# Kernel optimization log

Measured on AMD Instinct MI355X. Metric: run time of the kernel, lower is better.

## Reference

```python
import jax, jax.numpy as jnp
import numpy as np

B = 8192
D = 512          # hidden_dim
OBS_EMB = 256
COMM = 128
N_ACT = 4
N_LAYERS = 2
D_INNER = 2 * D
D_STATE = 16
DT_RANK = D // 16  # 32
D_CONV = 4
EPS = 1e-5


def _xavier(k, shape):
    s = jnp.sqrt(2.0 / (shape[-2] + shape[-1]))
    return jax.random.normal(k, shape, jnp.float32) * s


def setup_inputs() -> dict:
    ks = jax.random.split(jax.random.key(0), 16)
    p = {}
    p['obs'] = jax.random.normal(ks[0], (B, 75), jnp.float32)
    p['comm_in'] = jax.random.normal(ks[1], (B, COMM), jnp.float32)
    # obs encoder: Conv2d(3->32, k=3, valid) + Linear(288->256)
    p['conv_w'] = jax.random.normal(ks[2], (32, 3, 3, 3), jnp.float32) * jnp.sqrt(2.0 / 27.0)
    p['conv_b'] = jnp.zeros((32,), jnp.float32)
    p['enc_w'] = _xavier(ks[3], (288, OBS_EMB))
    p['enc_b'] = jnp.zeros((OBS_EMB,), jnp.float32)
    p['proj_w'] = _xavier(ks[4], (OBS_EMB + COMM, D))
    p['proj_b'] = jnp.zeros((D,), jnp.float32)
    # Mamba stack params (stacked over layers)
    p['norm_w'] = jnp.ones((N_LAYERS, D), jnp.float32)
    p['in_proj_w'] = _xavier(ks[5], (N_LAYERS, D, 2 * D_INNER))
    p['conv1d_w'] = jax.random.normal(ks[6], (N_LAYERS, D_INNER, D_CONV), jnp.float32) / jnp.sqrt(D_CONV)
    p['conv1d_b'] = jnp.zeros((N_LAYERS, D_INNER), jnp.float32)
    p['x_proj_w'] = _xavier(ks[7], (N_LAYERS, D_INNER, DT_RANK + 2 * D_STATE))
    p['dt_proj_w'] = _xavier(ks[8], (N_LAYERS, DT_RANK, D_INNER))
    p['dt_proj_b'] = jnp.full((N_LAYERS, D_INNER), jnp.log(jnp.expm1(0.01)), jnp.float32)  # dt ~ 0.01
    p['A_log'] = jnp.log(jnp.broadcast_to(jnp.arange(1, D_STATE + 1, dtype=jnp.float32), (N_LAYERS, D_INNER, D_STATE)))
    p['D_param'] = jnp.ones((N_LAYERS, D_INNER), jnp.float32)
    p['out_proj_w'] = _xavier(ks[9], (N_LAYERS, D_INNER, D))
    p['final_norm_w'] = jnp.ones((D,), jnp.float32)
    # output heads
    p['act_w'] = _xavier(ks[10], (D, N_ACT)); p['act_b'] = jnp.zeros((N_ACT,), jnp.float32)
    p['comm_w'] = _xavier(ks[11], (D, COMM)); p['comm_b'] = jnp.zeros((COMM,), jnp.float32)
    p['val_w'] = _xavier(ks[12], (D, 1)); p['val_b'] = jnp.zeros((1,), jnp.float32)
    return p


def _rmsnorm(x, w):
    return x * jax.lax.rsqrt(jnp.mean(x * x, axis=-1, keepdims=True) + EPS) * w


def _mamba_block(u, Wi, cw, cb, Wx, Wdt, bdt, Alog, Dp, Wo):
    # u: (B, L, D) -> (B, L, D)
    Bsz, L, _ = u.shape
    d_inner = Dp.shape[0]
    x, z = jnp.split(u @ Wi, 2, axis=-1)                       # (B,L,di) each
    # causal depthwise conv1d over L
    xt = jnp.pad(jnp.swapaxes(x, 1, 2), ((0, 0), (0, 0), (D_CONV - 1, 0)))
    xc = jax.lax.conv_general_dilated(xt, cw[:, None, :], (1,), 'VALID',
                                      feature_group_count=d_inner,
                                      dimension_numbers=('NCH', 'OIH', 'NCH'))
    x = jax.nn.silu(jnp.swapaxes(xc, 1, 2) + cb)
    x_dbl = x @ Wx                                              # (B,L,dt_rank+2*ns)
    dt = jax.nn.softplus(x_dbl[..., :DT_RANK] @ Wdt + bdt)      # (B,L,di)
    Bm = x_dbl[..., DT_RANK:DT_RANK + D_STATE]                  # (B,L,ns)
    Cm = x_dbl[..., DT_RANK + D_STATE:]                         # (B,L,ns)
    A = -jnp.exp(Alog)                                          # (di,ns)
    dA = jnp.exp(dt[..., None] * A)                             # (B,L,di,ns)
    dBx = dt[..., None] * Bm[:, :, None, :] * x[..., None]      # (B,L,di,ns)

    def step(h, inp):
        dA_t, dBx_t, C_t = inp
        h = dA_t * h + dBx_t
        return h, jnp.einsum('bds,bs->bd', h, C_t)

    h0 = jnp.zeros((Bsz, d_inner, D_STATE), u.dtype)
    _, ys = jax.lax.scan(step, h0, (jnp.swapaxes(dA, 0, 1), jnp.swapaxes(dBx, 0, 1), jnp.swapaxes(Cm, 0, 1)))
    y = jnp.swapaxes(ys, 0, 1) + x * Dp
    return (y * jax.nn.silu(z)) @ Wo


def reference(obs, comm_in, conv_w, conv_b, enc_w, enc_b, proj_w, proj_b,
              norm_w, in_proj_w, conv1d_w, conv1d_b, x_proj_w, dt_proj_w, dt_proj_b,
              A_log, D_param, out_proj_w, final_norm_w,
              act_w, act_b, comm_w, comm_b, val_w, val_b):
    Bsz = obs.shape[0]
    v = obs.reshape(Bsz, 3, 5, 5)
    v = jax.lax.conv_general_dilated(v, conv_w, (1, 1), 'VALID',
                                     dimension_numbers=('NCHW', 'OIHW', 'NCHW'))
    v = jax.nn.relu(v + conv_b[None, :, None, None]).reshape(Bsz, -1)   # (B,288)
    emb = jax.nn.relu(v @ enc_w + enc_b)                                 # (B,256)
    x = jax.nn.relu(jnp.concatenate([emb, comm_in], axis=-1) @ proj_w + proj_b)  # (B,512)
    h = x[:, None, :]                                                    # (B, L=1, D)
    for i in range(norm_w.shape[0]):
        h = h + _mamba_block(_rmsnorm(h, norm_w[i]), in_proj_w[i], conv1d_w[i],
                             conv1d_b[i], x_proj_w[i], dt_proj_w[i], dt_proj_b[i],
                             A_log[i], D_param[i], out_proj_w[i])
    h = _rmsnorm(h, final_norm_w)[:, 0, :]
    action_logits = h @ act_w + act_b
    comm_out = jnp.tanh(h @ comm_w + comm_b)
    value = h @ val_w + val_b
    return action_logits, comm_out, value
```

## Files before the change

kernel.cpp:

```cpp
#include <hip/hip_runtime.h>
#include <math.h>


typedef __bf16 bf16x8 __attribute__((ext_vector_type(8)));
typedef float f32x4 __attribute__((ext_vector_type(4)));
typedef short short8 __attribute__((ext_vector_type(8)));
typedef short short4v __attribute__((ext_vector_type(4)));

__device__ __forceinline__ float siluf(float v){ return v / (1.f + __expf(-v)); }
__device__ __forceinline__ float spfast(float v){ return v > 15.f ? v : __logf(1.f + __expf(v)); }
__device__ __forceinline__ float b2f(unsigned short u){ return __uint_as_float(((unsigned)u)<<16); }
__device__ __forceinline__ unsigned short f2b(float f){
  unsigned u = __float_as_uint(f);
  return (unsigned short)((u + 0x7fffu + ((u>>16)&1u)) >> 16);
}
__device__ __forceinline__ void g2l16(const void* g, void* l){
  __builtin_amdgcn_global_load_lds((const __attribute__((address_space(1))) unsigned int*)g,
                                   (__attribute__((address_space(3))) unsigned int*)l, 16, 0, 0);
}

__global__ __launch_bounds__(256) void k_wt_all(
    const float* __restrict__ in_proj_w, const float* __restrict__ out_proj_w,
    const float* __restrict__ x_proj_w,  const float* __restrict__ dt_proj_w,
    const float* __restrict__ enc_w,     const float* __restrict__ proj_w,
    const float* __restrict__ act_w, const float* __restrict__ comm_w, const float* __restrict__ val_w,
    const float* __restrict__ obs, const float* __restrict__ comm_in,
    const float* __restrict__ conv_w, const float* __restrict__ conv_b,
    unsigned short* __restrict__ wi_t, unsigned short* __restrict__ wo_t,
    unsigned short* __restrict__ wx_t, unsigned short* __restrict__ wdt_t,
    unsigned short* __restrict__ we_t, unsigned short* __restrict__ wp_t,
    unsigned short* __restrict__ wh_t,
    unsigned short* __restrict__ v, unsigned short* __restrict__ cat)
{
  int b = blockIdx.x;
  const int t = threadIdx.x;

  if (b >= 3792) {
    __shared__ float s_obs[8][76];
    const int r0 = (b - 3792) * 8;
    for (int i = t; i < 8*75; i += 256) s_obs[i/75][i%75] = obs[(size_t)(r0 + i/75)*75 + i%75];
    __syncthreads();
    for (int i = t; i < 8*288; i += 256) {
      int r = i / 288, o = i % 288;
      int c = o / 9, ij = o % 9, oi = ij/3, oj = ij%3;
      float acc = conv_b[c];
      #pragma unroll
      for (int ic=0; ic<3; ic++)
        #pragma unroll
        for (int ki=0; ki<3; ki++)
          #pragma unroll
          for (int kj=0; kj<3; kj++)
            acc = fmaf(s_obs[r][ic*25 + (oi+ki)*5 + (oj+kj)], conv_w[((c*3+ic)*3+ki)*3+kj], acc);
      v[(size_t)(r0+r)*320 + o] = f2b(fmaxf(acc, 0.f));
    }
    v[(size_t)(r0 + (t>>5))*320 + 288 + (t&31)] = 0;
    for (int i = t; i < 8*128; i += 256) {
      int r = i >> 7, c = i & 127;
      cat[(size_t)(r0+r)*384 + 256 + c] = f2b(comm_in[(size_t)(r0+r)*128 + c]);
    }
    return;
  }
  if (b >= 3536) {
    const int n = b - 3536;
    for (int k = t; k < 512; k += 256) {
      float v2;
      if (n < 4)         v2 = act_w[k*4 + n];
      else if (n < 132)  v2 = comm_w[k*128 + (n-4)];
      else if (n == 132) v2 = val_w[k];
      else               v2 = 0.f;
      wh_t[(size_t)n*512 + k] = f2b(v2);
    }
    return;
  }
  const float* Wsrc; unsigned short* Wdst; int Kd, Nd, KP, nkb;
  if (b < 2048) {
    const int L = b >> 10; b &= 1023;
    Wsrc = in_proj_w + (size_t)L*512*2048; Wdst = wi_t + (size_t)L*2048*512;
    Kd = 512; Nd = 2048; KP = 512; nkb = 16;
  } else if (b < 3072) {
    b -= 2048; const int L = b >> 9; b &= 511;
    Wsrc = out_proj_w + (size_t)L*1024*512; Wdst = wo_t + (size_t)L*512*1024;
    Kd = 1024; Nd = 512; KP = 1024; nkb = 32;
  } else if (b < 3200) {
    b -= 3072; const int L = b >> 6; b &= 63;
    Wsrc = x_proj_w + (size_t)L*1024*64; Wdst = wx_t + (size_t)L*64*1024;
    Kd = 1024; Nd = 64; KP = 1024; nkb = 32;
  } else if (b < 3264) {
    b -= 3200; const int L = b >> 5; b &= 31;
    Wsrc = dt_proj_w + (size_t)L*32*1024; Wdst = wdt_t + (size_t)L*1024*32;
    Kd = 32; Nd = 1024; KP = 32; nkb = 1;
  } else if (b < 3344) {
    b -= 3264; Wsrc = enc_w; Wdst = we_t; Kd = 288; Nd = 256; KP = 320; nkb = 10;
  } else {
    b -= 3344; Wsrc = proj_w; Wdst = wp_t; Kd = 384; Nd = 512; KP = 384; nkb = 12;
  }
  __shared__ float s[32][33];
  const int kb = (b % nkb)*32, nb = (b / nkb)*32;
  const int c = t & 31, r = t >> 5;
  #pragma unroll
  for (int i=0;i<32;i+=8) {
    const int k = kb + r + i;
    s[r+i][c] = (k < Kd) ? Wsrc[(size_t)k*Nd + nb + c] : 0.f;
  }
  __syncthreads();
  #pragma unroll
  for (int i=0;i<32;i+=8) Wdst[(size_t)(nb+r+i)*KP + kb + c] = f2b(s[c][r+i]);
}

__global__ __launch_bounds__(256) void k_rms(const float* __restrict__ h,
                                             const float* __restrict__ nw,
                                             unsigned short* __restrict__ u)
{
  const int l = threadIdx.x & 63;
  const size_t row = (size_t)blockIdx.x*4 + (threadIdx.x>>6);
  const float4* hp = (const float4*)(h + row*512) + l*2;
  float4 v0 = hp[0], v1 = hp[1];
  float ss = v0.x*v0.x+v0.y*v0.y+v0.z*v0.z+v0.w*v0.w
           + v1.x*v1.x+v1.y*v1.y+v1.z*v1.z+v1.w*v1.w;
  #pragma unroll
  for (int m=32;m;m>>=1) ss += __shfl_xor(ss, m, 64);
  const float sc = rsqrtf(ss*(1.f/512.f) + 1e-5f);
  const float4* np = (const float4*)nw + l*2;
  float4 w0 = np[0], w1 = np[1];
  short8 o;
  o[0]=(short)f2b(v0.x*sc*w0.x); o[1]=(short)f2b(v0.y*sc*w0.y);
  o[2]=(short)f2b(v0.z*sc*w0.z); o[3]=(short)f2b(v0.w*sc*w0.w);
  o[4]=(short)f2b(v1.x*sc*w1.x); o[5]=(short)f2b(v1.y*sc*w1.y);
  o[6]=(short)f2b(v1.z*sc*w1.z); o[7]=(short)f2b(v1.w*sc*w1.w);
  *(short8*)(u + row*512 + l*8) = o;
}

template<int K, int NB>
__device__ __forceinline__ void gemmT(const unsigned short* __restrict__ A,
                                      const unsigned short* __restrict__ Bt,
                                      int r0, int c0,
                                      unsigned short* sA, unsigned short* sB,
                                      f32x4 (&acc)[4][NB/32])
{
  constexpr int NF = NB/32;
  const int tid = threadIdx.x;
  const int l = tid & 63;
  const int wr = (tid>>7)&1, wc = (tid>>6)&1;
  const int rowA = tid>>3, kc8 = (tid&7)*8;
  const unsigned short* gA = A  + (size_t)(r0+rowA)*K + kc8;
  const unsigned short* gB = Bt + (size_t)(c0+rowA)*K + kc8;
  const int aOff = (wr*64 + (l&15))*64 + ((l>>4)*8);
  const int bOff = (wc*(NB/2) + (l&15))*64 + ((l>>4)*8);
  for (int kt=0; kt<K; kt+=64) {
    #pragma unroll
    for (int it=0; it<4; ++it) g2l16(gA + (size_t)(it*32)*K + kt, sA + ((it*256+tid)*8));
    #pragma unroll
    for (int it=0; it<NB/32; ++it) g2l16(gB + (size_t)(it*32)*K + kt, sB + ((it*256+tid)*8));
    __syncthreads();
    #pragma unroll
    for (int ks=0; ks<64; ks+=32) {
      bf16x8 af[4], bfm[NF];
      #pragma unroll
      for (int m=0;m<4;m++) af[m]  = *(const bf16x8*)(sA + (m*16)*64 + aOff + ks);
      #pragma unroll
      for (int n=0;n<NF;n++) bfm[n] = *(const bf16x8*)(sB + (n*16)*64 + bOff + ks);
      #pragma unroll
      for (int m=0;m<4;m++)
        #pragma unroll
        for (int n=0;n<NF;n++)
          acc[m][n] = __builtin_amdgcn_mfma_f32_16x16x32_bf16(af[m], bfm[n], acc[m][n], 0, 0, 0);
    }
    __syncthreads();
  }
}

__global__ __launch_bounds__(256) void k_gemm_inproj(
    const unsigned short* __restrict__ A, const unsigned short* __restrict__ Bt,
    const float* __restrict__ cw, const float* __restrict__ cb,
    unsigned short* __restrict__ xs, unsigned short* __restrict__ zs)
{
  __shared__ unsigned short sA[128*64], sB[128*64];
  f32x4 acc[4][4];
  #pragma unroll
  for (int m=0;m<4;m++)
    #pragma unroll
    for (int n=0;n<4;n++) acc[m][n] = (f32x4){0.f,0.f,0.f,0.f};
  const int r0 = blockIdx.x*128, c0 = blockIdx.y*128;
  gemmT<512,128>(A, Bt, r0, c0, sA, sB, acc);

  const int tid = threadIdx.x, l = tid & 63;
  const int wr = (tid>>7)&1, wc = (tid>>6)&1;
  const int colB = c0 + wc*64 + (l&15);
  const int rowB = r0 + wr*64 + ((l>>4)*4);
  if (c0 < 1024) {
    #pragma unroll
    for (int n=0;n<4;n++){
      const int col = colB + n*16;
      const float cw3 = cw[col*4+3], cbv = cb[col];
      #pragma unroll
      for (int m=0;m<4;m++)
        #pragma unroll
        for (int j=0;j<4;j++){
          const int row = rowB + m*16 + j;
          xs[(size_t)row*1024 + col] = f2b(siluf(fmaf(acc[m][n][j], cw3, cbv)));
        }
    }
  } else {
    #pragma unroll
    for (int n=0;n<4;n++){
      const int col = colB + n*16 - 1024;
      #pragma unroll
      for (int m=0;m<4;m++)
        #pragma unroll
        for (int j=0;j<4;j++){
          const int row = rowB + m*16 + j;
          zs[(size_t)row*1024 + col] = f2b(siluf(acc[m][n][j]));
        }
    }
  }
}

__global__ __launch_bounds__(256) void k_gemm_outproj(
    const unsigned short* __restrict__ A, const unsigned short* __restrict__ Bt,
    float* __restrict__ h)
{
  __shared__ unsigned short sA[128*64], sB[64*64];
  f32x4 acc[4][2];
  #pragma unroll
  for (int m=0;m<4;m++)
    #pragma unroll
    for (int n=0;n<2;n++) acc[m][n] = (f32x4){0.f,0.f,0.f,0.f};
  const int r0 = blockIdx.x*128, c0 = blockIdx.y*64;
  gemmT<1024,64>(A, Bt, r0, c0, sA, sB, acc);

  const int tid = threadIdx.x, l = tid & 63;
  const int wr = (tid>>7)&1, wc = (tid>>6)&1;
  const int colB = c0 + wc*32 + (l&15);
  const int rowB = r0 + wr*64 + ((l>>4)*4);
  #pragma unroll
  for (int n=0;n<2;n++){
    const int col = colB + n*16;
    #pragma unroll
    for (int m=0;m<4;m++)
      #pragma unroll
      for (int j=0;j<4;j++){
        const int row = rowB + m*16 + j;
        h[(size_t)row*512 + col] += acc[m][n][j];
      }
  }
}

__global__ __launch_bounds__(256) void k_gemm_enc(
    const unsigned short* __restrict__ A, const unsigned short* __restrict__ Bt,
    const float* __restrict__ bias, unsigned short* __restrict__ cat)
{
  __shared__ unsigned short sA[128*64], sB[64*64];
  f32x4 acc[4][2];
  #pragma unroll
  for (int m=0;m<4;m++)
    #pragma unroll
    for (int n=0;n<2;n++) acc[m][n] = (f32x4){0.f,0.f,0.f,0.f};
  const int r0 = blockIdx.x*128, c0 = blockIdx.y*64;
  gemmT<320,64>(A, Bt, r0, c0, sA, sB, acc);

  const int tid = threadIdx.x, l = tid & 63;
  const int wr = (tid>>7)&1, wc = (tid>>6)&1;
  const int colB = c0 + wc*32 + (l&15);
  const int rowB = r0 + wr*64 + ((l>>4)*4);
  #pragma unroll
  for (int n=0;n<2;n++){
    const int col = colB + n*16;
    const float bv = bias[col];
    #pragma unroll
    for (int m=0;m<4;m++)
      #pragma unroll
      for (int j=0;j<4;j++){
        const size_t row = rowB + m*16 + j;
        cat[row*384 + col] = f2b(fmaxf(acc[m][n][j] + bv, 0.f));
      }
  }
}

__global__ __launch_bounds__(256) void k_gemm_proj(
    const unsigned short* __restrict__ A, const unsigned short* __restrict__ Bt,
    const float* __restrict__ bias, float* __restrict__ h)
{
  __shared__ unsigned short sA[128*64], sB[64*64];
  f32x4 acc[4][2];
  #pragma unroll
  for (int m=0;m<4;m++)
    #pragma unroll
    for (int n=0;n<2;n++) acc[m][n] = (f32x4){0.f,0.f,0.f,0.f};
  const int r0 = blockIdx.x*128, c0 = blockIdx.y*64;
  gemmT<384,64>(A, Bt, r0, c0, sA, sB, acc);

  const int tid = threadIdx.x, l = tid & 63;
  const int wr = (tid>>7)&1, wc = (tid>>6)&1;
  const int colB = c0 + wc*32 + (l&15);
  const int rowB = r0 + wr*64 + ((l>>4)*4);
  #pragma unroll
  for (int n=0;n<2;n++){
    const int col = colB + n*16;
    const float bv = bias[col];
    #pragma unroll
    for (int m=0;m<4;m++)
      #pragma unroll
      for (int j=0;j<4;j++){
        const size_t row = rowB + m*16 + j;
        h[row*512 + col] = fmaxf(acc[m][n][j] + bv, 0.f);
      }
  }
}

__global__ __launch_bounds__(256) void k_gemm_heads(
    const unsigned short* __restrict__ A, const unsigned short* __restrict__ Bt,
    const float* __restrict__ act_b, const float* __restrict__ comm_b,
    const float* __restrict__ val_b, float* __restrict__ out)
{
  __shared__ unsigned short sA[128*64], sB[64*64];
  f32x4 acc[4][2];
  #pragma unroll
  for (int m=0;m<4;m++)
    #pragma unroll
    for (int n=0;n<2;n++) acc[m][n] = (f32x4){0.f,0.f,0.f,0.f};
  const int r0 = blockIdx.x*128, c0 = blockIdx.y*64;
  gemmT<512,64>(A, Bt, r0, c0, sA, sB, acc);

  const int tid = threadIdx.x, l = tid & 63;
  const int wr = (tid>>7)&1, wc = (tid>>6)&1;
  const int colB = c0 + wc*32 + (l&15);
  const int rowB = r0 + wr*64 + ((l>>4)*4);
  #pragma unroll
  for (int n=0;n<2;n++){
    const int col = colB + n*16;
    if (col > 132) continue;
    #pragma unroll
    for (int m=0;m<4;m++)
      #pragma unroll
      for (int j=0;j<4;j++){
        const size_t row = rowB + m*16 + j;
        float v = acc[m][n][j];
        if (col < 4)        out[row*4 + col] = v + act_b[col];
        else if (col < 132) out[32768 + row*128 + (col-4)] = tanhf(v + comm_b[col-4]);
        else                out[1081344 + row] = v + val_b[0];
      }
  }
}

__global__ __launch_bounds__(256) void k_xdbl2(
    const unsigned short* __restrict__ xs, const unsigned short* __restrict__ Wx_t,
    unsigned short* __restrict__ dt_in, float* __restrict__ bc_g)
{
  __shared__ unsigned short sA[32*128];
  __shared__ unsigned short sB[64*128];
  __shared__ float s_dbl[32][64];
  const int tid = threadIdx.x, l = tid & 63, w = tid >> 6;
  const int r0 = blockIdx.x * 32;
  f32x4 acc0 = (f32x4){0.f,0.f,0.f,0.f}, acc1 = (f32x4){0.f,0.f,0.f,0.f};
  for (int kt = 0; kt < 1024; kt += 128) {
    #pragma unroll
    for (int it=0; it<2; ++it) {
      const int idx = it*256 + tid;
      g2l16(xs + (size_t)(r0 + (idx>>4))*1024 + (idx&15)*8 + kt, sA + idx*8);
    }
    #pragma unroll
    for (int it=0; it<4; ++it) {
      const int idx = it*256 + tid;
      g2l16(Wx_t + (size_t)(idx>>4)*1024 + (idx&15)*8 + kt, sB + idx*8);
    }
    __syncthreads();
    #pragma unroll
    for (int ks=0; ks<128; ks+=32) {
      bf16x8 a0 = *(const bf16x8*)(sA + ((l&15))*128      + (l>>4)*8 + ks);
      bf16x8 a1 = *(const bf16x8*)(sA + (16+(l&15))*128   + (l>>4)*8 + ks);
      bf16x8 bf = *(const bf16x8*)(sB + (w*16+(l&15))*128 + (l>>4)*8 + ks);
      acc0 = __builtin_amdgcn_mfma_f32_16x16x32_bf16(a0, bf, acc0, 0, 0, 0);
      acc1 = __builtin_amdgcn_mfma_f32_16x16x32_bf16(a1, bf, acc1, 0, 0, 0);
    }
    __syncthreads();
  }
  #pragma unroll
  for (int j=0;j<4;j++) {
    s_dbl[(l>>4)*4 + j]     [w*16 + (l&15)] = acc0[j];
    s_dbl[16 + (l>>4)*4 + j][w*16 + (l&15)] = acc1[j];
  }
  __syncthreads();
  if (tid < 32) {
    float a = 0.f;
    #pragma unroll
    for (int s=0;s<16;s++) a = fmaf(s_dbl[tid][32+s], s_dbl[tid][48+s], a);
    bc_g[r0 + tid] = a;
  }
  {
    const int r = tid >> 3, c4 = (tid & 7)*4;
    short4v o;
    o[0] = (short)f2b(s_dbl[r][c4]);   o[1] = (short)f2b(s_dbl[r][c4+1]);
    o[2] = (short)f2b(s_dbl[r][c4+2]); o[3] = (short)f2b(s_dbl[r][c4+3]);
    *(short4v*)(dt_in + (size_t)(r0+r)*32 + c4) = o;
  }
}

__global__ __launch_bounds__(256) void k_dtgate2(
    unsigned short* __restrict__ xs, const unsigned short* __restrict__ zs,
    const unsigned short* __restrict__ dt_in, const float* __restrict__ bc_g,
    const unsigned short* __restrict__ Wdt_t,
    const float* __restrict__ bdt, const float* __restrict__ Dp)
{
  __shared__ unsigned short sA[128*32];
  __shared__ unsigned short sB[128*32];
  __shared__ float s_bc[128];
  const int tid = threadIdx.x, l = tid & 63;
  const int r0 = blockIdx.x*128, c0 = blockIdx.y*128;

  { const int row = tid >> 1, kh = (tid & 1)*16;
    const short8* ap = (const short8*)(dt_in + (size_t)(r0+row)*32 + kh);
    *(short8*)(sA + row*32 + kh)     = ap[0];
    *(short8*)(sA + row*32 + kh + 8) = ap[1];
    const short8* wp = (const short8*)(Wdt_t + (size_t)(c0+row)*32 + kh);
    *(short8*)(sB + row*32 + kh)     = wp[0];
    *(short8*)(sB + row*32 + kh + 8) = wp[1];
  }
  if (tid < 128) s_bc[tid] = bc_g[r0 + tid];
  __syncthreads();

  const int wr = (tid>>7)&1, wc = (tid>>6)&1;
  bf16x8 af[4], bfm[4];
  #pragma unroll
  for (int m=0;m<4;m++) af[m]  = *(const bf16x8*)(sA + (wr*64 + m*16 + (l&15))*32 + (l>>4)*8);
  #pragma unroll
  for (int n=0;n<4;n++) bfm[n] = *(const bf16x8*)(sB + (wc*64 + n*16 + (l&15))*32 + (l>>4)*8);
  f32x4 acc[4][4];
  #pragma unroll
  for (int m=0;m<4;m++)
    #pragma unroll
    for (int n=0;n<4;n++)
      acc[m][n] = __builtin_amdgcn_mfma_f32_16x16x32_bf16(af[m], bfm[n], (f32x4){0.f,0.f,0.f,0.f}, 0, 0, 0);

  #pragma unroll
  for (int n=0;n<4;n++){
    const int col = c0 + wc*64 + n*16 + (l&15);
    const float bj = bdt[col], dpj = Dp[col];
    #pragma unroll
    for (int m=0;m<4;m++){
      const int rloc = wr*64 + m*16 + (l>>4)*4;
      #pragma unroll
      for (int j=0;j<4;j++){
        const size_t row = r0 + rloc + j;
        const float dtv = spfast(acc[m][n][j] + bj);
        const float f = fmaf(dtv, s_bc[rloc + j], dpj);
        const float x = b2f(xs[row*1024 + col]);
        const float z = b2f(zs[row*1024 + col]);
        xs[row*1024 + col] = f2b(x * f * z);
      }
    }
  }
}

extern "C" void kernel_launch(void* const* d_in, const int* in_sizes, int n_in,
                              void* d_out, int out_size, void* d_ws, size_t ws_size,
                              hipStream_t stream) {
  const float* obs       = (const float*)d_in[0];
  const float* comm_in   = (const float*)d_in[1];
  const float* conv_w    = (const float*)d_in[2];
  const float* conv_b    = (const float*)d_in[3];
  const float* enc_w     = (const float*)d_in[4];
  const float* enc_b     = (const float*)d_in[5];
  const float* proj_w    = (const float*)d_in[6];
  const float* proj_b    = (const float*)d_in[7];
  const float* norm_w    = (const float*)d_in[8];
  const float* in_proj_w = (const float*)d_in[9];
  const float* conv1d_w  = (const float*)d_in[10];
  const float* conv1d_b  = (const float*)d_in[11];
  const float* x_proj_w  = (const float*)d_in[12];
  const float* dt_proj_w = (const float*)d_in[13];
  const float* dt_proj_b = (const float*)d_in[14];
  const float* D_param   = (const float*)d_in[16];
  const float* out_proj_w= (const float*)d_in[17];
  const float* final_nw  = (const float*)d_in[18];
  const float* act_w     = (const float*)d_in[19];
  const float* act_b     = (const float*)d_in[20];
  const float* comm_w    = (const float*)d_in[21];
  const float* comm_b    = (const float*)d_in[22];
  const float* val_w     = (const float*)d_in[23];
  const float* val_b     = (const float*)d_in[24];
  float* out = (float*)d_out;

  char* W = (char*)d_ws;
  float* h             = (float*)W;
  unsigned short* u_b  = (unsigned short*)(W + (16u<<20));
  unsigned short* xs_b = (unsigned short*)(W + (24u<<20));
  unsigned short* zs_b = (unsigned short*)(W + (40u<<20));
  unsigned short* wi_t = (unsigned short*)(W + (56u<<20));
  unsigned short* wo_t = (unsigned short*)(W + (60u<<20));
  unsigned short* dt_in= (unsigned short*)(W + (62u<<20));
  float* bc_g          = (float*)(W + (62u<<20) + (512u<<10));
  unsigned short* wx_t = (unsigned short*)(W + (64u<<20));
  unsigned short* wdt_t= (unsigned short*)(W + (64u<<20) + (256u<<10));
  unsigned short* wh_t = (unsigned short*)(W + (65u<<20));
  unsigned short* we_t = (unsigned short*)(W + (65u<<20) + (512u<<10));
  unsigned short* wp_t = (unsigned short*)(W + (66u<<20));

  unsigned short* v_b   = xs_b;
  unsigned short* cat_b = zs_b;

  k_wt_all<<<4816,256,0,stream>>>(in_proj_w, out_proj_w, x_proj_w, dt_proj_w,
                                  enc_w, proj_w, act_w, comm_w, val_w,
                                  obs, comm_in, conv_w, conv_b,
                                  wi_t, wo_t, wx_t, wdt_t, we_t, wp_t, wh_t,
                                  v_b, cat_b);

  k_gemm_enc<<<dim3(64,4),256,0,stream>>>(v_b, we_t, enc_b, cat_b);
  k_gemm_proj<<<dim3(64,8),256,0,stream>>>(cat_b, wp_t, proj_b, h);

  for (int L=0; L<2; L++) {
    k_rms<<<2048,256,0,stream>>>(h, norm_w + L*512, u_b);
    k_gemm_inproj<<<dim3(64,16),256,0,stream>>>(u_b, wi_t + (size_t)L*2048*512,
                                                conv1d_w + L*1024*4, conv1d_b + L*1024, xs_b, zs_b);
    k_xdbl2<<<256,256,0,stream>>>(xs_b, wx_t + (size_t)L*64*1024, dt_in, bc_g);
    k_dtgate2<<<dim3(64,8),256,0,stream>>>(xs_b, zs_b, dt_in, bc_g, wdt_t + (size_t)L*1024*32,
                                           dt_proj_b + L*1024, D_param + L*1024);
    k_gemm_outproj<<<dim3(64,8),256,0,stream>>>(xs_b, wo_t + (size_t)L*512*1024, h);
  }
  k_rms<<<2048,256,0,stream>>>(h, final_nw, u_b);
  k_gemm_heads<<<dim3(64,4),256,0,stream>>>(u_b, wh_t, act_b, comm_b, val_b, out);
}
```

Before: 253.7 us.

## Fuse x_proj and dt-gate kernels, enlarge in_proj tile to 256 rows

Merges the x_proj GEMM and the dt_proj/gating kernel into one kernel per 32-row block. The block keeps the full xs row slab in LDS and reuses it for both the x_proj GEMM and the gating. This drops the dt_in/bc_g round trip through global memory and one kernel launch per layer. The in_proj GEMM also moves to 512-thread blocks with 256-row tiles to improve weight reuse. The costs are a large LDS footprint (about 64KB for sX), which limits occupancy, and only 256 blocks for the fused kernel.

```diff
diff --git a/kernel.cpp b/kernel.cpp
--- a/kernel.cpp
+++ b/kernel.cpp
@@ -5,7 +5,6 @@
 typedef __bf16 bf16x8 __attribute__((ext_vector_type(8)));
 typedef float f32x4 __attribute__((ext_vector_type(4)));
 typedef short short8 __attribute__((ext_vector_type(8)));
-typedef short short4v __attribute__((ext_vector_type(4)));
 
 __device__ __forceinline__ float siluf(float v){ return v / (1.f + __expf(-v)); }
 __device__ __forceinline__ float spfast(float v){ return v > 15.f ? v : __logf(1.f + __expf(v)); }
@@ -169,22 +168,46 @@
   }
 }
 
-__global__ __launch_bounds__(256) void k_gemm_inproj(
+__global__ __launch_bounds__(512) void k_gemm_inproj(
     const unsigned short* __restrict__ A, const unsigned short* __restrict__ Bt,
     const float* __restrict__ cw, const float* __restrict__ cb,
     unsigned short* __restrict__ xs, unsigned short* __restrict__ zs)
 {
-  __shared__ unsigned short sA[128*64], sB[128*64];
+  __shared__ unsigned short sA[256*64], sB[128*64];
   f32x4 acc[4][4];
   #pragma unroll
   for (int m=0;m<4;m++)
     #pragma unroll
     for (int n=0;n<4;n++) acc[m][n] = (f32x4){0.f,0.f,0.f,0.f};
-  const int r0 = blockIdx.x*128, c0 = blockIdx.y*128;
-  gemmT<512,128>(A, Bt, r0, c0, sA, sB, acc);
-
   const int tid = threadIdx.x, l = tid & 63;
-  const int wr = (tid>>7)&1, wc = (tid>>6)&1;
+  const int w = tid >> 6, wr = w >> 1, wc = w & 1;
+  const int r0 = blockIdx.x*256, c0 = blockIdx.y*128;
+  const int rowA = tid>>3, kc8 = (tid&7)*8;
+  const unsigned short* gA = A  + (size_t)(r0+rowA)*512 + kc8;
+  const unsigned short* gB = Bt + (size_t)(c0+rowA)*512 + kc8;
+  const int aOff = (wr*64 + (l&15))*64 + ((l>>4)*8);
+  const int bOff = (wc*64 + (l&15))*64 + ((l>>4)*8);
+  for (int kt=0; kt<512; kt+=64) {
+    #pragma unroll
+    for (int it=0; it<4; ++it) g2l16(gA + (size_t)(it*64)*512 + kt, sA + ((it*512+tid)*8));
+    #pragma unroll
+    for (int it=0; it<2; ++it) g2l16(gB + (size_t)(it*64)*512 + kt, sB + ((it*512+tid)*8));
+    __syncthreads();
+    #pragma unroll
+    for (int ks=0; ks<64; ks+=32) {
+      bf16x8 af[4], bfm[4];
+      #pragma unroll
+      for (int m=0;m<4;m++) af[m]  = *(const bf16x8*)(sA + (m*16)*64 + aOff + ks);
+      #pragma unroll
+      for (int n=0;n<4;n++) bfm[n] = *(const bf16x8*)(sB + (n*16)*64 + bOff + ks);
+      #pragma unroll
+      for (int m=0;m<4;m++)
+        #pragma unroll
+        for (int n=0;n<4;n++)
+          acc[m][n] = __builtin_amdgcn_mfma_f32_16x16x32_bf16(af[m], bfm[n], acc[m][n], 0, 0, 0);
+    }
+    __syncthreads();
+  }
   const int colB = c0 + wc*64 + (l&15);
   const int rowB = r0 + wr*64 + ((l>>4)*4);
   if (c0 < 1024) {
@@ -342,22 +365,27 @@
   }
 }
 
-__global__ __launch_bounds__(256) void k_xdbl2(
-    const unsigned short* __restrict__ xs, const unsigned short* __restrict__ Wx_t,
-    unsigned short* __restrict__ dt_in, float* __restrict__ bc_g)
-{
-  __shared__ unsigned short sA[32*128];
+__global__ __launch_bounds__(256) void k_ssm_f(
+    unsigned short* __restrict__ xs, const unsigned short* __restrict__ zs,
+    const unsigned short* __restrict__ Wx_t, const unsigned short* __restrict__ Wdt_t,
+    const float* __restrict__ bdt, const float* __restrict__ Dp)
+{
+  __shared__ unsigned short sX[32*1024];
   __shared__ unsigned short sB[64*128];
   __shared__ float s_dbl[32][64];
+  __shared__ unsigned short sDt[32*32];
+  __shared__ float s_bc[32];
   const int tid = threadIdx.x, l = tid & 63, w = tid >> 6;
   const int r0 = blockIdx.x * 32;
+
+  #pragma unroll
+  for (int it=0; it<16; ++it) {
+    const int idx = it*256 + tid;
+    g2l16(xs + (size_t)(r0 + (idx>>7))*1024 + (idx&127)*8, sX + idx*8);
+  }
+
   f32x4 acc0 = (f32x4){0.f,0.f,0.f,0.f}, acc1 = (f32x4){0.f,0.f,0.f,0.f};
   for (int kt = 0; kt < 1024; kt += 128) {
-    #pragma unroll
-    for (int it=0; it<2; ++it) {
-      const int idx = it*256 + tid;
-      g2l16(xs + (size_t)(r0 + (idx>>4))*1024 + (idx&15)*8 + kt, sA + idx*8);
-    }
     #pragma unroll
     for (int it=0; it<4; ++it) {
       const int idx = it*256 + tid;
@@ -366,8 +394,8 @@
     __syncthreads();
     #pragma unroll
     for (int ks=0; ks<128; ks+=32) {
-      bf16x8 a0 = *(const bf16x8*)(sA + ((l&15))*128      + (l>>4)*8 + ks);
-      bf16x8 a1 = *(const bf16x8*)(sA + (16+(l&15))*128   + (l>>4)*8 + ks);
+      bf16x8 a0 = *(const bf16x8*)(sX + ((l&15))*1024    + (l>>4)*8 + kt + ks);
+      bf16x8 a1 = *(const bf16x8*)(sX + (16+(l&15))*1024 + (l>>4)*8 + kt + ks);
       bf16x8 bf = *(const bf16x8*)(sB + (w*16+(l&15))*128 + (l>>4)*8 + ks);
       acc0 = __builtin_amdgcn_mfma_f32_16x16x32_bf16(a0, bf, acc0, 0, 0, 0);
       acc1 = __builtin_amdgcn_mfma_f32_16x16x32_bf16(a1, bf, acc1, 0, 0, 0);
@@ -384,70 +412,53 @@
     float a = 0.f;
     #pragma unroll
     for (int s=0;s<16;s++) a = fmaf(s_dbl[tid][32+s], s_dbl[tid][48+s], a);
-    bc_g[r0 + tid] = a;
+    s_bc[tid] = a;
   }
   {
     const int r = tid >> 3, c4 = (tid & 7)*4;
-    short4v o;
-    o[0] = (short)f2b(s_dbl[r][c4]);   o[1] = (short)f2b(s_dbl[r][c4+1]);
-    o[2] = (short)f2b(s_dbl[r][c4+2]); o[3] = (short)f2b(s_dbl[r][c4+3]);
-    *(short4v*)(dt_in + (size_t)(r0+r)*32 + c4) = o;
-  }
-}
-
-__global__ __launch_bounds__(256) void k_dtgate2(
-    unsigned short* __restrict__ xs, const unsigned short* __restrict__ zs,
-    const unsigned short* __restrict__ dt_in, const float* __restrict__ bc_g,
-    const unsigned short* __restrict__ Wdt_t,
-    const float* __restrict__ bdt, const float* __restrict__ Dp)
-{
-  __shared__ unsigned short sA[128*32];
-  __shared__ unsigned short sB[128*32];
-  __shared__ float s_bc[128];
-  const int tid = threadIdx.x, l = tid & 63;
-  const int r0 = blockIdx.x*128, c0 = blockIdx.y*128;
-
-  { const int row = tid >> 1, kh = (tid & 1)*16;
-    const short8* ap = (const short8*)(dt_in + (size_t)(r0+row)*32 + kh);
-    *(short8*)(sA + row*32 + kh)     = ap[0];
-    *(short8*)(sA + row*32 + kh + 8) = ap[1];
-    const short8* wp = (const short8*)(Wdt_t + (size_t)(c0+row)*32 + kh);
-    *(short8*)(sB + row*32 + kh)     = wp[0];
-    *(short8*)(sB + row*32 + kh + 8) = wp[1];
-  }
-  if (tid < 128) s_bc[tid] = bc_g[r0 + tid];
+    sDt[r*32 + c4]   = f2b(s_dbl[r][c4]);
+    sDt[r*32 + c4+1] = f2b(s_dbl[r][c4+1]);
+    sDt[r*32 + c4+2] = f2b(s_dbl[r][c4+2]);
+    sDt[r*32 + c4+3] = f2b(s_dbl[r][c4+3]);
+  }
   __syncthreads();
 
-  const int wr = (tid>>7)&1, wc = (tid>>6)&1;
-  bf16x8 af[4], bfm[4];
-  #pragma unroll
-  for (int m=0;m<4;m++) af[m]  = *(const bf16x8*)(sA + (wr*64 + m*16 + (l&15))*32 + (l>>4)*8);
-  #pragma unroll
-  for (int n=0;n<4;n++) bfm[n] = *(const bf16x8*)(sB + (wc*64 + n*16 + (l&15))*32 + (l>>4)*8);
-  f32x4 acc[4][4];
-  #pragma unroll
-  for (int m=0;m<4;m++)
-    #pragma unroll
-    for (int n=0;n<4;n++)
-      acc[m][n] = __builtin_amdgcn_mfma_f32_16x16x32_bf16(af[m], bfm[n], (f32x4){0.f,0.f,0.f,0.f}, 0, 0, 0);
-
-  #pragma unroll
-  for (int n=0;n<4;n++){
-    const int col = c0 + wc*64 + n*16 + (l&15);
-    const float bj = bdt[col], dpj = Dp[col];
-    #pragma unroll
-    for (int m=0;m<4;m++){
-      const int rloc = wr*64 + m*16 + (l>>4)*4;
-      #pragma unroll
-      for (int j=0;j<4;j++){
-        const size_t row = r0 + rloc + j;
-        const float dtv = spfast(acc[m][n][j] + bj);
-        const float f = fmaf(dtv, s_bc[rloc + j], dpj);
-        const float x = b2f(xs[row*1024 + col]);
-        const float z = b2f(zs[row*1024 + col]);
-        xs[row*1024 + col] = f2b(x * f * z);
+  bf16x8 af0 = *(const bf16x8*)(sDt + ((l&15))*32    + (l>>4)*8);
+  bf16x8 af1 = *(const bf16x8*)(sDt + (16+(l&15))*32 + (l>>4)*8);
+  for (int c = 0; c < 4; ++c) {
+    const int cc = c*256;
+    #pragma unroll
+    for (int it=0; it<4; ++it) {
+      const int idx = it*256 + tid;
+      g2l16(Wdt_t + (size_t)(cc + (idx>>2))*32 + (idx&3)*8, sB + idx*8);
+    }
+    __syncthreads();
+    f32x4 a2[2][4];
+    #pragma unroll
+    for (int n=0;n<4;n++){
+      bf16x8 bn = *(const bf16x8*)(sB + (w*64 + n*16 + (l&15))*32 + (l>>4)*8);
+      a2[0][n] = __builtin_amdgcn_mfma_f32_16x16x32_bf16(af0, bn, (f32x4){0.f,0.f,0.f,0.f}, 0, 0, 0);
+      a2[1][n] = __builtin_amdgcn_mfma_f32_16x16x32_bf16(af1, bn, (f32x4){0.f,0.f,0.f,0.f}, 0, 0, 0);
+    }
+    #pragma unroll
+    for (int n=0;n<4;n++){
+      const int col = cc + w*64 + n*16 + (l&15);
+      const float bj = bdt[col], dpj = Dp[col];
+      #pragma unroll
+      for (int m=0;m<2;m++){
+        #pragma unroll
+        for (int j=0;j<4;j++){
+          const int rloc = m*16 + (l>>4)*4 + j;
+          const size_t row = r0 + rloc;
+          const float dtv = spfast(a2[m][n][j] + bj);
+          const float f = fmaf(dtv, s_bc[rloc], dpj);
+          const float x = b2f(sX[rloc*1024 + col]);
+          const float z = b2f(zs[row*1024 + col]);
+          xs[row*1024 + col] = f2b(x * f * z);
+        }
       }
     }
+    __syncthreads();
   }
 }
 
@@ -487,8 +498,6 @@
   unsigned short* zs_b = (unsigned short*)(W + (40u<<20));
   unsigned short* wi_t = (unsigned short*)(W + (56u<<20));
   unsigned short* wo_t = (unsigned short*)(W + (60u<<20));
-  unsigned short* dt_in= (unsigned short*)(W + (62u<<20));
-  float* bc_g          = (float*)(W + (62u<<20) + (512u<<10));
   unsigned short* wx_t = (unsigned short*)(W + (64u<<20));
   unsigned short* wdt_t= (unsigned short*)(W + (64u<<20) + (256u<<10));
   unsigned short* wh_t = (unsigned short*)(W + (65u<<20));
@@ -509,11 +518,11 @@
 
   for (int L=0; L<2; L++) {
     k_rms<<<2048,256,0,stream>>>(h, norm_w + L*512, u_b);
-    k_gemm_inproj<<<dim3(64,16),256,0,stream>>>(u_b, wi_t + (size_t)L*2048*512,
+    k_gemm_inproj<<<dim3(32,16),512,0,stream>>>(u_b, wi_t + (size_t)L*2048*512,
                                                 conv1d_w + L*1024*4, conv1d_b + L*1024, xs_b, zs_b);
-    k_xdbl2<<<256,256,0,stream>>>(xs_b, wx_t + (size_t)L*64*1024, dt_in, bc_g);
-    k_dtgate2<<<dim3(64,8),256,0,stream>>>(xs_b, zs_b, dt_in, bc_g, wdt_t + (size_t)L*1024*32,
-                                           dt_proj_b + L*1024, D_param + L*1024);
+    k_ssm_f<<<256,256,0,stream>>>(xs_b, zs_b, wx_t + (size_t)L*64*1024,
+                                  wdt_t + (size_t)L*1024*32,
+                                  dt_proj_b + L*1024, D_param + L*1024);
     k_gemm_outproj<<<dim3(64,8),256,0,stream>>>(xs_b, wo_t + (size_t)L*512*1024, h);
   }
   k_rms<<<2048,256,0,stream>>>(h, final_nw, u_b);
```

New measurement: 256.2 us. Within noise of the previous version (+1.0%).
